# Kernel optimization log

Measured on AMD Instinct MI355X. Metric: run time of the kernel, lower is better.

## Reference

```python
import jax, jax.numpy as jnp
import numpy as np

N_HEADS = 12
HEAD_DIM = 64
EMB_DIM = 768
ATTN_DIM = N_HEADS * HEAD_DIM


def setup_inputs() -> dict:
    key = jax.random.key(0)
    k1, k2, k3, k4 = jax.random.split(key, 4)
    B, N = 8, 1024
    x = jax.random.normal(k1, (B, N, EMB_DIM), dtype=jnp.float32)
    scale = 1.0 / np.sqrt(EMB_DIM)
    w_qkv = jax.random.normal(k2, (EMB_DIM, 3 * ATTN_DIM), dtype=jnp.float32) * scale
    w_out = jax.random.normal(k3, (ATTN_DIM, EMB_DIM), dtype=jnp.float32) * (1.0 / np.sqrt(ATTN_DIM))
    b_out = jax.random.normal(k4, (EMB_DIM,), dtype=jnp.float32) * 0.01
    return {"x": x, "w_qkv": w_qkv, "w_out": w_out, "b_out": b_out}


def reference(x, w_qkv, w_out, b_out):
    B, N, _ = x.shape
    qkv = jnp.einsum('bnd,de->bne', x, w_qkv)  # [B,N,3*attn_dim]
    q, k, v = jnp.split(qkv, 3, axis=-1)
    # [B, n_heads, N, head_dim]
    def heads(t):
        return t.reshape(B, N, N_HEADS, HEAD_DIM).transpose(0, 2, 1, 3)
    q, k, v = heads(q), heads(k), heads(v)
    scores = jnp.einsum('bhnd,bhmd->bhnm', q, k) * (HEAD_DIM ** -0.5)
    attn = jax.nn.softmax(scores, axis=-1)
    out = jnp.einsum('bhnm,bhmd->bhnd', attn, v)
    out = out.transpose(0, 2, 1, 3).reshape(B, N, ATTN_DIM)
    return jnp.einsum('bnd,de->bne', out, w_out) + b_out
```

## Files before the change

### kernel.cpp

```cpp
#include <hip/hip_runtime.h>
#include <hip/hip_bf16.h>

typedef unsigned short u16;
typedef __attribute__((ext_vector_type(8))) short short8;
typedef __attribute__((ext_vector_type(4))) float floatx4;

#define SEQ    1024
#define EMB    768
#define NHEADS 12
#define HDIM   64
#define QKVD   2304
#define BATCH  8
#define ROWS   8192
#define QKW    1536

__device__ __forceinline__ u16 f2bf(float f) {
  unsigned int x; __builtin_memcpy(&x, &f, 4);
  x = (x + 0x7FFFu + ((x >> 16) & 1u)) >> 16;
  return (u16)x;
}
__device__ __forceinline__ unsigned int pack2bf_t(float a, float b) {
  unsigned int ua, ub;
  __builtin_memcpy(&ua, &a, 4); __builtin_memcpy(&ub, &b, 4);
  return (ub & 0xFFFF0000u) | (ua >> 16);
}

__device__ __forceinline__ void gld16(const void* g, void* l) {
  __builtin_amdgcn_global_load_lds(
      (const __attribute__((address_space(1))) void*)g,
      (__attribute__((address_space(3))) void*)l, 16, 0, 0);
}

#define PIPE_BARRIER_VM(N) asm volatile("s_waitcnt vmcnt(" #N ")\n\ts_barrier" ::: "memory")
#define PIPE_BARRIER       asm volatile("s_barrier" ::: "memory")

__global__ __launch_bounds__(256) void f2bf_vec(const float* __restrict__ src,
                                                u16* __restrict__ dst, int n) {
  const int i = (blockIdx.x * 256 + threadIdx.x) * 8;
  if (i >= n) return;
  u16 tmp[8];
#pragma unroll
  for (int j = 0; j < 8; ++j) tmp[j] = f2bf(src[i + j]);
  *(uint4*)(dst + i) = *(const uint4*)tmp;
}

__global__ __launch_bounds__(256) void transpose_w(const float* __restrict__ wqkv,
                                                   const float* __restrict__ wout,
                                                   u16* __restrict__ dqkv,
                                                   u16* __restrict__ dout) {
  __shared__ u16 tile[32][33];
  const bool second = blockIdx.x >= 72;
  const float* in = second ? wout : wqkv;
  u16* out = second ? dout : dqkv;
  const int C = second ? EMB : QKVD;
  const int bx = second ? blockIdx.x - 72 : blockIdx.x;
  const int c0 = bx * 32, r0 = blockIdx.y * 32;
  const int tx = threadIdx.x, ty = threadIdx.y;
#pragma unroll
  for (int i = 0; i < 4; ++i)
    tile[ty + i * 8][tx] = f2bf(in[(size_t)(r0 + ty + i * 8) * C + c0 + tx]);
  __syncthreads();
#pragma unroll
  for (int i = 0; i < 4; ++i)
    out[(size_t)(c0 + ty + i * 8) * EMB + r0 + tx] = tile[tx][ty + i * 8];
}

__global__ __launch_bounds__(256) void gemm_qkv(const u16* __restrict__ A,
                                                const u16* __restrict__ Bt,
                                                u16* __restrict__ qk,
                                                u16* __restrict__ vT) {
  constexpr int K = EMB, ITERS = K / 64;
  __shared__ __align__(16) u16 As[2][128 * 64];
  __shared__ __align__(16) u16 Bs[2][128 * 64];
  const int t = threadIdx.x;
  const int w = t >> 6, lane = t & 63, l16 = lane & 15, quad = lane >> 4;
  const int wm = (w >> 1) * 64, wn = (w & 1) * 64;
  const int flat = blockIdx.y * 18 + blockIdx.x;
  const int grp = flat / 144, loc = flat % 144;
  const int m0 = (grp * 8 + (loc & 7)) * 128;
  const int n0 = (loc >> 3) * 128;

  auto stage = [&](int k0, int buf) {
#pragma unroll
    for (int i = 0; i < 4; ++i) {
      const int idx = i * 256 + t;
      const int row = idx >> 3;
      const int gc8 = (((idx & 7) ^ (row & 7)) << 3);
      gld16(A  + (size_t)(m0 + row) * K + k0 + gc8, &As[buf][(size_t)idx * 8]);
      gld16(Bt + (size_t)(n0 + row) * K + k0 + gc8, &Bs[buf][(size_t)idx * 8]);
    }
  };

  floatx4 acc[4][4];
#pragma unroll
  for (int mt = 0; mt < 4; ++mt)
#pragma unroll
    for (int nt = 0; nt < 4; ++nt) acc[mt][nt] = (floatx4){0.f, 0.f, 0.f, 0.f};

  stage(0, 0);
  for (int it = 0; it < ITERS; ++it) {
    const int cur = it & 1;
    if (it + 1 < ITERS) {
      stage((it + 1) * 64, cur ^ 1);
      PIPE_BARRIER_VM(8);
    } else {
      PIPE_BARRIER_VM(0);
    }
#pragma unroll
    for (int kk = 0; kk < 2; ++kk) {
      short8 a[4], b[4];
#pragma unroll
      for (int mt = 0; mt < 4; ++mt) {
        const int row = wm + mt * 16 + l16;
        a[mt] = *(const short8*)(&As[cur][row * 64 + ((((kk << 2) + quad) ^ (row & 7)) << 3)]);
      }
#pragma unroll
      for (int nt = 0; nt < 4; ++nt) {
        const int row = wn + nt * 16 + l16;
        b[nt] = *(const short8*)(&Bs[cur][row * 64 + ((((kk << 2) + quad) ^ (row & 7)) << 3)]);
      }
#pragma unroll
      for (int mt = 0; mt < 4; ++mt)
#pragma unroll
        for (int nt = 0; nt < 4; ++nt)
          acc[mt][nt] = __builtin_amdgcn_mfma_f32_16x16x32_bf16(a[mt], b[nt], acc[mt][nt], 0, 0, 0);
    }
    PIPE_BARRIER;
  }

  if (n0 < QKW) {
#pragma unroll
    for (int mt = 0; mt < 4; ++mt)
#pragma unroll
      for (int nt = 0; nt < 4; ++nt) {
        const int col = n0 + wn + nt * 16 + l16;
#pragma unroll
        for (int r = 0; r < 4; ++r) {
          const int row = m0 + wm + mt * 16 + quad * 4 + r;
          qk[(size_t)row * QKW + col] = f2bf(acc[mt][nt][r]);
        }
      }
  } else {
#pragma unroll
    for (int mt = 0; mt < 4; ++mt) {
      const int rowb = m0 + wm + mt * 16 + quad * 4;
      const int b = rowb >> 10, n = rowb & 1023;
#pragma unroll
      for (int nt = 0; nt < 4; ++nt) {
        const int vc = n0 + wn + nt * 16 + l16 - QKW;
        const int h = vc >> 6, d = vc & 63;
        ushort4 pk;
        pk.x = f2bf(acc[mt][nt][0]); pk.y = f2bf(acc[mt][nt][1]);
        pk.z = f2bf(acc[mt][nt][2]); pk.w = f2bf(acc[mt][nt][3]);
        *(ushort4*)(vT + ((size_t)(b * NHEADS + h) * HDIM + d) * SEQ + n) = pk;
      }
    }
  }
}

__global__ __launch_bounds__(256) void flash_attn(const u16* __restrict__ qk,
                                                  const u16* __restrict__ vT,
                                                  u16* __restrict__ aout) {
  __shared__ __align__(16) u16 QPs[128 * 64];
  __shared__ __align__(16) u16 Ks[2][64 * 64];
  __shared__ __align__(16) u16 Vs[2][64 * 64];

  const int t = threadIdx.x;
  const int w = t >> 6, lane = t & 63, l16 = lane & 15, quad = lane >> 4;
  const int bh = blockIdx.x, b = bh / NHEADS, h = bh % NHEADS;
  const int m0 = blockIdx.y * 128;
  constexpr float C_EXP = 0.125f * 1.44269504f;
  constexpr int ITERS = SEQ / 64;

  const size_t kbase = (size_t)(b * SEQ) * QKW + EMB + h * HDIM;
  const size_t vbase = (size_t)bh * HDIM * SEQ;

  auto stage = [&](int n0, int buf) {
#pragma unroll
    for (int i = 0; i < 2; ++i) {
      const int idx = i * 256 + t, kr = idx >> 3;
      const int gc = (((idx & 7) ^ (kr & 7)) << 3);
      gld16(qk + kbase + (size_t)(n0 + kr) * QKW + gc, &Ks[buf][(size_t)idx * 8]);
      gld16(vT + vbase + (size_t)kr * SEQ + n0 + gc,   &Vs[buf][(size_t)idx * 8]);
    }
  };

  stage(0, 0);

  const size_t qbase = (size_t)(b * SEQ + m0) * QKW + h * HDIM;
#pragma unroll
  for (int i = 0; i < 4; ++i) {
    const int idx = i * 256 + t, row = idx >> 3, c = idx & 7;
    *(uint4*)(QPs + row * 64 + ((c ^ (row & 7)) << 3)) =
        *(const uint4*)(qk + qbase + (size_t)row * QKW + (c << 3));
  }
  __syncthreads();

  short8 bq[2][2];
#pragma unroll
  for (int mt = 0; mt < 2; ++mt)
#pragma unroll
    for (int kc = 0; kc < 2; ++kc)
      bq[mt][kc] = *(const short8*)(QPs + (w * 32 + mt * 16 + l16) * 64 +
                                    ((((kc << 2) + quad) ^ (l16 & 7)) << 3));

  float l_r[2] = {0.f, 0.f};
  floatx4 o[2][4];
#pragma unroll
  for (int mt = 0; mt < 2; ++mt)
#pragma unroll
    for (int ct = 0; ct < 4; ++ct) o[mt][ct] = (floatx4){0.f, 0.f, 0.f, 0.f};

  u16* Pw = QPs + w * 32 * 64;

  for (int it = 0; it < ITERS; ++it) {
    const int cur = it & 1;
    if (it + 1 < ITERS) {
      stage((it + 1) * 64, cur ^ 1);
      PIPE_BARRIER_VM(4);
    } else {
      PIPE_BARRIER_VM(0);
    }

    floatx4 st[4][2];
#pragma unroll
    for (int kt = 0; kt < 4; ++kt)
#pragma unroll
      for (int mt = 0; mt < 2; ++mt) st[kt][mt] = (floatx4){0.f, 0.f, 0.f, 0.f};
#pragma unroll
    for (int kt = 0; kt < 4; ++kt) {
      const int krow = (kt * 16 + l16) * 64;
      const short8 ak0 = *(const short8*)(&Ks[cur][krow + (((0 + quad) ^ (l16 & 7)) << 3)]);
      const short8 ak1 = *(const short8*)(&Ks[cur][krow + (((4 + quad) ^ (l16 & 7)) << 3)]);
#pragma unroll
      for (int mt = 0; mt < 2; ++mt) {
        st[kt][mt] = __builtin_amdgcn_mfma_f32_16x16x32_bf16(ak0, bq[mt][0], st[kt][mt], 0, 0, 0);
        st[kt][mt] = __builtin_amdgcn_mfma_f32_16x16x32_bf16(ak1, bq[mt][1], st[kt][mt], 0, 0, 0);
      }
    }

#pragma unroll
    for (int mt = 0; mt < 2; ++mt) {
      float lacc = 0.f;
#pragma unroll
      for (int kt = 0; kt < 4; ++kt) {
        const float p0 = __builtin_amdgcn_exp2f(st[kt][mt][0] * C_EXP);
        const float p1 = __builtin_amdgcn_exp2f(st[kt][mt][1] * C_EXP);
        const float p2 = __builtin_amdgcn_exp2f(st[kt][mt][2] * C_EXP);
        const float p3 = __builtin_amdgcn_exp2f(st[kt][mt][3] * C_EXP);
        lacc += (p0 + p1) + (p2 + p3);
        uint2 pw2;
        pw2.x = pack2bf_t(p0, p1);
        pw2.y = pack2bf_t(p2, p3);
        *(uint2*)(Pw + (mt * 16 + l16) * 64 +
                  ((((kt << 1) + (quad >> 1)) ^ (l16 & 7)) << 3) + (quad & 1) * 4) = pw2;
      }
      l_r[mt] += lacc;
    }

#pragma unroll
    for (int kk = 0; kk < 2; ++kk) {
      const int sl = (((kk << 2) + quad) ^ (l16 & 7)) << 3;
      const short8 ap0 = *(const short8*)(Pw + (0 * 16 + l16) * 64 + sl);
      const short8 ap1 = *(const short8*)(Pw + (1 * 16 + l16) * 64 + sl);
#pragma unroll
      for (int ct = 0; ct < 4; ++ct) {
        const short8 bv = *(const short8*)(&Vs[cur][(ct * 16 + l16) * 64 + sl]);
        o[0][ct] = __builtin_amdgcn_mfma_f32_16x16x32_bf16(ap0, bv, o[0][ct], 0, 0, 0);
        o[1][ct] = __builtin_amdgcn_mfma_f32_16x16x32_bf16(ap1, bv, o[1][ct], 0, 0, 0);
      }
    }
    PIPE_BARRIER;
  }

  float invs[2][4];
#pragma unroll
  for (int mt = 0; mt < 2; ++mt) {
    float l = l_r[mt];
    l += __shfl_xor(l, 16);
    l += __shfl_xor(l, 32);
    const float iv = 1.f / l;
#pragma unroll
    for (int r = 0; r < 4; ++r) invs[mt][r] = __shfl(iv, quad * 4 + r);
  }
#pragma unroll
  for (int mt = 0; mt < 2; ++mt)
#pragma unroll
    for (int ct = 0; ct < 4; ++ct)
#pragma unroll
      for (int r = 0; r < 4; ++r) {
        const int row = m0 + w * 32 + mt * 16 + quad * 4 + r;
        const int col = h * HDIM + ct * 16 + l16;
        aout[(size_t)(b * SEQ + row) * EMB + col] = f2bf(o[mt][ct][r] * invs[mt][r]);
      }
}

__global__ __launch_bounds__(256) void gemm_out(const u16* __restrict__ A,
                                                const u16* __restrict__ Bt,
                                                const float* __restrict__ bias,
                                                float* __restrict__ C) {
  constexpr int K = EMB, N = EMB, ITERS = K / 64;
  __shared__ __align__(16) u16 As[2][64 * 64];
  __shared__ __align__(16) u16 Bs[2][128 * 64];
  const int t = threadIdx.x;
  const int w = t >> 6, lane = t & 63, l16 = lane & 15, quad = lane >> 4;
  const int wm = (w >> 1) * 32, wn = (w & 1) * 64;
  const int flat = blockIdx.y * 6 + blockIdx.x;
  const int grp = flat / 48, loc = flat % 48;
  const int m0 = (grp * 8 + (loc & 7)) * 64;
  const int n0 = (loc >> 3) * 128;

  auto stage = [&](int k0, int buf) {
#pragma unroll
    for (int i = 0; i < 2; ++i) {
      const int idx = i * 256 + t;
      const int row = idx >> 3;
      const int gc8 = (((idx & 7) ^ (row & 7)) << 3);
      gld16(A + (size_t)(m0 + row) * K + k0 + gc8, &As[buf][(size_t)idx * 8]);
    }
#pragma unroll
    for (int i = 0; i < 4; ++i) {
      const int idx = i * 256 + t;
      const int row = idx >> 3;
      const int gc8 = (((idx & 7) ^ (row & 7)) << 3);
      gld16(Bt + (size_t)(n0 + row) * K + k0 + gc8, &Bs[buf][(size_t)idx * 8]);
    }
  };

  floatx4 acc[2][4];
#pragma unroll
  for (int mt = 0; mt < 2; ++mt)
#pragma unroll
    for (int nt = 0; nt < 4; ++nt) acc[mt][nt] = (floatx4){0.f, 0.f, 0.f, 0.f};

  stage(0, 0);
  for (int it = 0; it < ITERS; ++it) {
    const int cur = it & 1;
    if (it + 1 < ITERS) {
      stage((it + 1) * 64, cur ^ 1);
      PIPE_BARRIER_VM(6);
    } else {
      PIPE_BARRIER_VM(0);
    }
#pragma unroll
    for (int kk = 0; kk < 2; ++kk) {
      short8 a[2], b[4];
#pragma unroll
      for (int mt = 0; mt < 2; ++mt) {
        const int row = wm + mt * 16 + l16;
        a[mt] = *(const short8*)(&As[cur][row * 64 + ((((kk << 2) + quad) ^ (row & 7)) << 3)]);
      }
#pragma unroll
      for (int nt = 0; nt < 4; ++nt) {
        const int row = wn + nt * 16 + l16;
        b[nt] = *(const short8*)(&Bs[cur][row * 64 + ((((kk << 2) + quad) ^ (row & 7)) << 3)]);
      }
#pragma unroll
      for (int mt = 0; mt < 2; ++mt)
#pragma unroll
        for (int nt = 0; nt < 4; ++nt)
          acc[mt][nt] = __builtin_amdgcn_mfma_f32_16x16x32_bf16(a[mt], b[nt], acc[mt][nt], 0, 0, 0);
    }
    PIPE_BARRIER;
  }

#pragma unroll
  for (int mt = 0; mt < 2; ++mt)
#pragma unroll
    for (int nt = 0; nt < 4; ++nt) {
      const int col = n0 + wn + nt * 16 + l16;
      const float badd = bias[col];
#pragma unroll
      for (int r = 0; r < 4; ++r) {
        const int row = m0 + wm + mt * 16 + quad * 4 + r;
        C[(size_t)row * N + col] = acc[mt][nt][r] + badd;
      }
    }
}

extern "C" void kernel_launch(void* const* d_in, const int* in_sizes, int n_in,
                              void* d_out, int out_size, void* d_ws, size_t ws_size,
                              hipStream_t stream) {
  const float* x     = (const float*)d_in[0];
  const float* w_qkv = (const float*)d_in[1];
  const float* w_out = (const float*)d_in[2];
  const float* b_out = (const float*)d_in[3];
  float* out = (float*)d_out;

  u16* qk    = (u16*)d_ws;
  u16* vT    = qk    + (size_t)ROWS * QKW;
  u16* xb    = vT    + (size_t)BATCH * NHEADS * HDIM * SEQ;
  u16* aout  = xb;
  u16* wqkvT = xb    + (size_t)ROWS * EMB;
  u16* woutT = wqkvT + (size_t)QKVD * EMB;

  f2bf_vec<<<ROWS * EMB / 8 / 256, 256, 0, stream>>>(x, xb, ROWS * EMB);
  transpose_w<<<dim3(96, 24), dim3(32, 8), 0, stream>>>(w_qkv, w_out, wqkvT, woutT);

  gemm_qkv<<<dim3(18, 64), 256, 0, stream>>>(xb, wqkvT, qk, vT);

  flash_attn<<<dim3(BATCH * NHEADS, SEQ / 128), 256, 0, stream>>>(qk, vT, aout);

  gemm_out<<<dim3(6, 128), 256, 0, stream>>>(aout, woutT, b_out, out);
}
```

Baseline: 179.9 us.

## Fuse prep kernels, triple-buffer 32-key attention tiles, compute row sums via MFMA

Merges the x-to-bf16 conversion and weight transpose into one prep launch to save a kernel launch. The flash attention loop now uses 32-key tiles with a three-stage load pipeline (two tiles prefetched ahead) instead of 64-key double buffering. Softmax row sums are computed with an MFMA against a ones vector, replacing the scalar adds and shuffles. This trades more loop iterations and barriers for deeper prefetch and less VALU work, and sums now use bf16-rounded probabilities.

```diff
diff --git a/kernel.cpp b/kernel.cpp
--- a/kernel.cpp
+++ b/kernel.cpp
@@ -34,28 +34,30 @@
 #define PIPE_BARRIER_VM(N) asm volatile("s_waitcnt vmcnt(" #N ")\n\ts_barrier" ::: "memory")
 #define PIPE_BARRIER       asm volatile("s_barrier" ::: "memory")
 
-__global__ __launch_bounds__(256) void f2bf_vec(const float* __restrict__ src,
-                                                u16* __restrict__ dst, int n) {
-  const int i = (blockIdx.x * 256 + threadIdx.x) * 8;
-  if (i >= n) return;
-  u16 tmp[8];
-#pragma unroll
-  for (int j = 0; j < 8; ++j) tmp[j] = f2bf(src[i + j]);
-  *(uint4*)(dst + i) = *(const uint4*)tmp;
-}
-
-__global__ __launch_bounds__(256) void transpose_w(const float* __restrict__ wqkv,
-                                                   const float* __restrict__ wout,
-                                                   u16* __restrict__ dqkv,
-                                                   u16* __restrict__ dout) {
+__global__ __launch_bounds__(256) void prep(const float* __restrict__ x,
+                                            const float* __restrict__ wqkv,
+                                            const float* __restrict__ wout,
+                                            u16* __restrict__ xb,
+                                            u16* __restrict__ dqkv,
+                                            u16* __restrict__ dout) {
+  const int t = threadIdx.x;
+  if (blockIdx.x < 3072) {
+    const int i = (blockIdx.x * 256 + t) * 8;
+    u16 tmp[8];
+#pragma unroll
+    for (int j = 0; j < 8; ++j) tmp[j] = f2bf(x[i + j]);
+    *(uint4*)(xb + i) = *(const uint4*)tmp;
+    return;
+  }
   __shared__ u16 tile[32][33];
-  const bool second = blockIdx.x >= 72;
+  const int bid = blockIdx.x - 3072;
+  const int bx = bid % 96, by = bid / 96;
+  const bool second = bx >= 72;
   const float* in = second ? wout : wqkv;
   u16* out = second ? dout : dqkv;
   const int C = second ? EMB : QKVD;
-  const int bx = second ? blockIdx.x - 72 : blockIdx.x;
-  const int c0 = bx * 32, r0 = blockIdx.y * 32;
-  const int tx = threadIdx.x, ty = threadIdx.y;
+  const int c0 = (second ? bx - 72 : bx) * 32, r0 = by * 32;
+  const int tx = t & 31, ty = t >> 5;
 #pragma unroll
   for (int i = 0; i < 4; ++i)
     tile[ty + i * 8][tx] = f2bf(in[(size_t)(r0 + ty + i * 8) * C + c0 + tx]);
@@ -162,30 +164,30 @@
                                                   const u16* __restrict__ vT,
                                                   u16* __restrict__ aout) {
   __shared__ __align__(16) u16 QPs[128 * 64];
-  __shared__ __align__(16) u16 Ks[2][64 * 64];
-  __shared__ __align__(16) u16 Vs[2][64 * 64];
+  __shared__ __align__(16) u16 Ks[3][32 * 64];
+  __shared__ __align__(16) u16 Vs[3][64 * 32];
 
   const int t = threadIdx.x;
   const int w = t >> 6, lane = t & 63, l16 = lane & 15, quad = lane >> 4;
   const int bh = blockIdx.x, b = bh / NHEADS, h = bh % NHEADS;
   const int m0 = blockIdx.y * 128;
   constexpr float C_EXP = 0.125f * 1.44269504f;
-  constexpr int ITERS = SEQ / 64;
+  constexpr int ITERS = SEQ / 32;
 
   const size_t kbase = (size_t)(b * SEQ) * QKW + EMB + h * HDIM;
   const size_t vbase = (size_t)bh * HDIM * SEQ;
 
   auto stage = [&](int n0, int buf) {
-#pragma unroll
-    for (int i = 0; i < 2; ++i) {
-      const int idx = i * 256 + t, kr = idx >> 3;
-      const int gc = (((idx & 7) ^ (kr & 7)) << 3);
-      gld16(qk + kbase + (size_t)(n0 + kr) * QKW + gc, &Ks[buf][(size_t)idx * 8]);
-      gld16(vT + vbase + (size_t)kr * SEQ + n0 + gc,   &Vs[buf][(size_t)idx * 8]);
-    }
+    const int kr = t >> 3, ck = t & 7;
+    gld16(qk + kbase + (size_t)(n0 + kr) * QKW + ((ck ^ (kr & 7)) << 3),
+          &Ks[buf][(size_t)t * 8]);
+    const int dr = t >> 2, cv = t & 3;
+    gld16(vT + vbase + (size_t)dr * SEQ + n0 + ((cv ^ (dr & 3)) << 3),
+          &Vs[buf][(size_t)t * 8]);
   };
 
   stage(0, 0);
+  stage(32, 1);
 
   const size_t qbase = (size_t)(b * SEQ + m0) * QKW + h * HDIM;
 #pragma unroll
@@ -204,31 +206,39 @@
       bq[mt][kc] = *(const short8*)(QPs + (w * 32 + mt * 16 + l16) * 64 +
                                     ((((kc << 2) + quad) ^ (l16 & 7)) << 3));
 
-  float l_r[2] = {0.f, 0.f};
-  floatx4 o[2][4];
-#pragma unroll
-  for (int mt = 0; mt < 2; ++mt)
+  short8 ones;
+#pragma unroll
+  for (int j = 0; j < 8; ++j) ones[j] = (short)0x3F80;
+
+  floatx4 o[2][4], lcc[2];
+#pragma unroll
+  for (int mt = 0; mt < 2; ++mt) {
+    lcc[mt] = (floatx4){0.f, 0.f, 0.f, 0.f};
 #pragma unroll
     for (int ct = 0; ct < 4; ++ct) o[mt][ct] = (floatx4){0.f, 0.f, 0.f, 0.f};
+  }
 
   u16* Pw = QPs + w * 32 * 64;
 
+  int cur = 0;
   for (int it = 0; it < ITERS; ++it) {
-    const int cur = it & 1;
-    if (it + 1 < ITERS) {
-      stage((it + 1) * 64, cur ^ 1);
+    int nxt = cur + 2; if (nxt >= 3) nxt -= 3;
+    if (it + 2 < ITERS) {
+      stage((it + 2) * 32, nxt);
       PIPE_BARRIER_VM(4);
+    } else if (it + 1 < ITERS) {
+      PIPE_BARRIER_VM(2);
     } else {
       PIPE_BARRIER_VM(0);
     }
 
-    floatx4 st[4][2];
-#pragma unroll
-    for (int kt = 0; kt < 4; ++kt)
+    floatx4 st[2][2];
+#pragma unroll
+    for (int kt = 0; kt < 2; ++kt)
 #pragma unroll
       for (int mt = 0; mt < 2; ++mt) st[kt][mt] = (floatx4){0.f, 0.f, 0.f, 0.f};
 #pragma unroll
-    for (int kt = 0; kt < 4; ++kt) {
+    for (int kt = 0; kt < 2; ++kt) {
       const int krow = (kt * 16 + l16) * 64;
       const short8 ak0 = *(const short8*)(&Ks[cur][krow + (((0 + quad) ^ (l16 & 7)) << 3)]);
       const short8 ak1 = *(const short8*)(&Ks[cur][krow + (((4 + quad) ^ (l16 & 7)) << 3)]);
@@ -240,59 +250,50 @@
     }
 
 #pragma unroll
-    for (int mt = 0; mt < 2; ++mt) {
-      float lacc = 0.f;
-#pragma unroll
-      for (int kt = 0; kt < 4; ++kt) {
+    for (int mt = 0; mt < 2; ++mt)
+#pragma unroll
+      for (int kt = 0; kt < 2; ++kt) {
         const float p0 = __builtin_amdgcn_exp2f(st[kt][mt][0] * C_EXP);
         const float p1 = __builtin_amdgcn_exp2f(st[kt][mt][1] * C_EXP);
         const float p2 = __builtin_amdgcn_exp2f(st[kt][mt][2] * C_EXP);
         const float p3 = __builtin_amdgcn_exp2f(st[kt][mt][3] * C_EXP);
-        lacc += (p0 + p1) + (p2 + p3);
         uint2 pw2;
         pw2.x = pack2bf_t(p0, p1);
         pw2.y = pack2bf_t(p2, p3);
         *(uint2*)(Pw + (mt * 16 + l16) * 64 +
-                  ((((kt << 1) + (quad >> 1)) ^ (l16 & 7)) << 3) + (quad & 1) * 4) = pw2;
-      }
-      l_r[mt] += lacc;
-    }
-
-#pragma unroll
-    for (int kk = 0; kk < 2; ++kk) {
-      const int sl = (((kk << 2) + quad) ^ (l16 & 7)) << 3;
-      const short8 ap0 = *(const short8*)(Pw + (0 * 16 + l16) * 64 + sl);
-      const short8 ap1 = *(const short8*)(Pw + (1 * 16 + l16) * 64 + sl);
+                  ((((kt << 1) + (quad >> 1)) ^ (l16 & 7)) << 3) + ((quad & 1) << 2)) = pw2;
+      }
+
+#pragma unroll
+    for (int mt = 0; mt < 2; ++mt) {
+      const short8 ap = *(const short8*)(Pw + (mt * 16 + l16) * 64 +
+                                        ((quad ^ (l16 & 7)) << 3));
+      lcc[mt] = __builtin_amdgcn_mfma_f32_16x16x32_bf16(ap, ones, lcc[mt], 0, 0, 0);
 #pragma unroll
       for (int ct = 0; ct < 4; ++ct) {
-        const short8 bv = *(const short8*)(&Vs[cur][(ct * 16 + l16) * 64 + sl]);
-        o[0][ct] = __builtin_amdgcn_mfma_f32_16x16x32_bf16(ap0, bv, o[0][ct], 0, 0, 0);
-        o[1][ct] = __builtin_amdgcn_mfma_f32_16x16x32_bf16(ap1, bv, o[1][ct], 0, 0, 0);
+        const short8 bv = *(const short8*)(&Vs[cur][(ct * 16 + l16) * 32 +
+                                                    ((quad ^ (l16 & 3)) << 3)]);
+        o[mt][ct] = __builtin_amdgcn_mfma_f32_16x16x32_bf16(ap, bv, o[mt][ct], 0, 0, 0);
       }
     }
     PIPE_BARRIER;
-  }
-
-  float invs[2][4];
+    cur = (cur + 1 == 3) ? 0 : cur + 1;
+  }
+
 #pragma unroll
   for (int mt = 0; mt < 2; ++mt) {
-    float l = l_r[mt];
-    l += __shfl_xor(l, 16);
-    l += __shfl_xor(l, 32);
-    const float iv = 1.f / l;
-#pragma unroll
-    for (int r = 0; r < 4; ++r) invs[mt][r] = __shfl(iv, quad * 4 + r);
-  }
-#pragma unroll
-  for (int mt = 0; mt < 2; ++mt)
+    floatx4 inv;
+#pragma unroll
+    for (int r = 0; r < 4; ++r) inv[r] = 1.f / lcc[mt][r];
 #pragma unroll
     for (int ct = 0; ct < 4; ++ct)
 #pragma unroll
       for (int r = 0; r < 4; ++r) {
         const int row = m0 + w * 32 + mt * 16 + quad * 4 + r;
         const int col = h * HDIM + ct * 16 + l16;
-        aout[(size_t)(b * SEQ + row) * EMB + col] = f2bf(o[mt][ct][r] * invs[mt][r]);
-      }
+        aout[(size_t)(b * SEQ + row) * EMB + col] = f2bf(o[mt][ct][r] * inv[r]);
+      }
+  }
 }
 
 __global__ __launch_bounds__(256) void gemm_out(const u16* __restrict__ A,
@@ -394,8 +395,7 @@
   u16* wqkvT = xb    + (size_t)ROWS * EMB;
   u16* woutT = wqkvT + (size_t)QKVD * EMB;
 
-  f2bf_vec<<<ROWS * EMB / 8 / 256, 256, 0, stream>>>(x, xb, ROWS * EMB);
-  transpose_w<<<dim3(96, 24), dim3(32, 8), 0, stream>>>(w_qkv, w_out, wqkvT, woutT);
+  prep<<<3072 + 2304, 256, 0, stream>>>(x, w_qkv, w_out, xb, wqkvT, woutT);
 
   gemm_qkv<<<dim3(18, 64), 256, 0, stream>>>(xb, wqkvT, qk, vT);
 
```

After: 187.2 us. 4.1% more time.
